# Optimization experiments

Hardware: AMD Instinct MI355X
Metric: run time of the kernel (lower is better)

## Reference

```python
import jax, jax.numpy as jnp
import numpy as np

B, C, P, NP = 16, 768, 2048, 64
FFE = 4


def _ln(x, g, b, eps=1e-5):
    m = jnp.mean(x, axis=-1, keepdims=True)
    v = jnp.mean(jnp.square(x - m), axis=-1, keepdims=True)
    return (x - m) * jax.lax.rsqrt(v + eps) * g + b


def _gelu(x):
    return jax.nn.gelu(x, approximate=False)  # torch nn.GELU default (erf)


def _any_attn(q, k, v, nqg, nqb, nkg, nkb, nvg, nvb, wq, wk, wv, wp, bq, bk, bv, bp):
    # AnyAttention: LN each stream, project, ReLU-gated logits scaled by d^-0.5, softmax, proj
    scale = q.shape[-1] ** -0.5
    qn = _ln(q, nqg, nqb) @ wq + bq
    kn = _ln(k, nkg, nkb) @ wk + bk
    vn = _ln(v, nvg, nvb) @ wv + bv
    attn = jnp.einsum('bqc,bkc->bqk', qn, kn)
    attn = jax.nn.relu(attn) * scale  # returned attn is relu*scale (pre-softmax)
    out = jnp.einsum('bqk,bkc->bqc', jax.nn.softmax(attn, axis=-1), vn)
    return attn, out @ wp + bp


def _forward(x, parts,
             enc_nq_g, enc_nq_b, enc_nk_g, enc_nk_b, enc_nv_g, enc_nv_b,
             enc_wq, enc_wk, enc_wv, enc_wp, enc_bq, enc_bk, enc_bv, enc_bp,
             dec_nq_g, dec_nq_b, dec_nk_g, dec_nk_b, dec_nv_g, dec_nv_b,
             dec_wq, dec_wk, dec_wv, dec_wp, dec_bq, dec_bk, dec_bv, dec_bp,
             ffn_ng, ffn_nb, ffn_w1, ffn_b1, ffn_w2, ffn_b2,
             sr_w1, sr_b1, sr_w2, sr_b2):
    x = jnp.swapaxes(x, 1, 2)  # b c p -> b p c
    # SimpleReasoning: SE-style gate over part tokens (AdaptiveMaxPool1d(1) = max over channel dim)
    g = jnp.max(parts, axis=-1)                                  # [b, np]
    g = _gelu(g @ sr_w1 + sr_b1)
    gate = jax.nn.sigmoid(g @ sr_w2 + sr_b2)[..., None]          # [b, np, 1]
    parts = gate * parts + parts                                 # parts1 + parts (residual)
    # enc_attn: parts attend over image tokens
    attn0, attn_out = _any_attn(parts, x, x,
                                enc_nq_g, enc_nq_b, enc_nk_g, enc_nk_b, enc_nv_g, enc_nv_b,
                                enc_wq, enc_wk, enc_wv, enc_wp, enc_bq, enc_bk, enc_bv, enc_bp)
    attn_0 = jnp.max(attn0, axis=-1)                             # maxpool over k -> [b, np]
    parts_in = parts + attn_out
    # FFN on image tokens with residual
    h = _ln(x, ffn_ng, ffn_nb)
    feats1 = x + (_gelu(h @ ffn_w1 + ffn_b1) @ ffn_w2 + ffn_b2)
    # dec_attn: image tokens attend over part tokens
    _, feats = _any_attn(feats1, parts_in, parts_in,
                         dec_nq_g, dec_nq_b, dec_nk_g, dec_nk_b, dec_nv_g, dec_nv_b,
                         dec_wq, dec_wk, dec_wv, dec_wp, dec_bq, dec_bk, dec_bv, dec_bp)
    feats = x + feats
    return jnp.swapaxes(feats, 1, 2), attn_0                     # [b, c, p], [b, np]


def setup_inputs() -> dict:
    key = jax.random.key(0)
    ki = iter(jax.random.split(key, 48))
    def rn(shape, s=1.0):
        return jax.random.normal(next(ki), shape, jnp.float32) * s
    d = {}
    d['x'] = rn((B, C, P))
    d['parts'] = rn((B, NP, C))
    for pre in ('enc', 'dec'):
        for nm in ('nq', 'nk', 'nv'):
            d[f'{pre}_{nm}_g'] = jnp.ones((C,), jnp.float32)
            d[f'{pre}_{nm}_b'] = jnp.zeros((C,), jnp.float32)
        for nm in ('wq', 'wk', 'wv', 'wp'):
            d[f'{pre}_{nm}'] = rn((C, C), 0.02)
        for nm in ('bq', 'bk', 'bv', 'bp'):
            d[f'{pre}_{nm}'] = jnp.zeros((C,), jnp.float32)
    d['ffn_ng'] = jnp.ones((C,), jnp.float32)
    d['ffn_nb'] = jnp.zeros((C,), jnp.float32)
    d['ffn_w1'] = rn((C, FFE * C), 0.02)
    d['ffn_b1'] = jnp.zeros((FFE * C,), jnp.float32)
    d['ffn_w2'] = rn((FFE * C, C), 0.02)
    d['ffn_b2'] = jnp.zeros((C,), jnp.float32)
    d['sr_w1'] = rn((NP, NP), 0.1)
    d['sr_b1'] = jnp.zeros((NP,), jnp.float32)
    d['sr_w2'] = rn((NP, NP), 0.1)
    d['sr_b2'] = jnp.zeros((NP,), jnp.float32)
    return d


def reference(x, parts,
              enc_nq_g, enc_nq_b, enc_nk_g, enc_nk_b, enc_nv_g, enc_nv_b,
              enc_wq, enc_wk, enc_wv, enc_wp, enc_bq, enc_bk, enc_bv, enc_bp,
              dec_nq_g, dec_nq_b, dec_nk_g, dec_nk_b, dec_nv_g, dec_nv_b,
              dec_wq, dec_wk, dec_wv, dec_wp, dec_bq, dec_bk, dec_bv, dec_bp,
              ffn_ng, ffn_nb, ffn_w1, ffn_b1, ffn_w2, ffn_b2,
              sr_w1, sr_b1, sr_w2, sr_b2):
    return _forward(x, parts,
                    enc_nq_g, enc_nq_b, enc_nk_g, enc_nk_b, enc_nv_g, enc_nv_b,
                    enc_wq, enc_wk, enc_wv, enc_wp, enc_bq, enc_bk, enc_bv, enc_bp,
                    dec_nq_g, dec_nq_b, dec_nk_g, dec_nk_b, dec_nv_g, dec_nv_b,
                    dec_wq, dec_wk, dec_wv, dec_wp, dec_bq, dec_bk, dec_bv, dec_bp,
                    ffn_ng, ffn_nb, ffn_w1, ffn_b1, ffn_w2, ffn_b2,
                    sr_w1, sr_b1, sr_w2, sr_b2)
```

## Files before the change

### kernel.cpp

```cpp
#include <hip/hip_runtime.h>

typedef unsigned short u16;
typedef unsigned int u32;
typedef __bf16 bf16x8 __attribute__((ext_vector_type(8)));
typedef float f32x4 __attribute__((ext_vector_type(4)));
typedef unsigned int u32x4 __attribute__((ext_vector_type(4)));

#define BB 16
#define CC 768
#define PP 2048
#define FF 3072

__device__ __forceinline__ float b2f(u16 u) {
  unsigned int x = ((unsigned int)u) << 16;
  return __builtin_bit_cast(float, x);
}
__device__ __forceinline__ u16 f2b(float f) {
  unsigned int x = __builtin_bit_cast(unsigned int, f);
  x += 0x7fffu + ((x >> 16) & 1u);
  return (u16)(x >> 16);
}
__device__ __forceinline__ float erf_fast(float x) {
  float ax = fabsf(x);
  float t = 1.0f / fmaf(0.3275911f, ax, 1.0f);
  float p = t * fmaf(t, fmaf(t, fmaf(t, fmaf(t, 1.061405429f, -1.453152027f),
                                     1.421413741f), -0.284496736f), 0.254829592f);
  float r = 1.0f - p * __expf(-ax * ax);
  return copysignf(r, x);
}
__device__ __forceinline__ float gelu_f(float x) {
  return 0.5f * x * (1.0f + erf_fast(x * 0.7071067811865475f));
}

typedef __attribute__((address_space(1))) const unsigned int g_u32;
typedef __attribute__((address_space(3))) unsigned int l_u32;
__device__ __forceinline__ void gl_lds16(const u16* g, u16* l) {
  __builtin_amdgcn_global_load_lds((g_u32*)g, (l_u32*)l, 16, 0, 0);
}

struct Wtr10 {
  const float* W[10]; const float* g[10]; u16* O[10];
  int Kd[10]; int Nd[10]; int tr[10]; int cum[11];
};
__global__ void wtr10_k(Wtr10 a) {
  __shared__ float t[64][65];
  int tbid = blockIdx.x;
  int z = 0;
  while (tbid >= a.cum[z + 1]) ++z;
  int r = tbid - a.cum[z];
  const float* W = a.W[z];
  const float* g = a.g[z];
  u16* Wt = a.O[z];
  int K = a.Kd[z], N = a.Nd[z];
  int nbx = N >> 6;
  int n0 = (r % nbx) * 64, k0 = (r / nbx) * 64;
  int tx = threadIdx.x & 63, ty = threadIdx.x >> 6;
  if (!a.tr[z]) {
    for (int i = 0; i < 16; ++i) {
      int k = k0 + ty + i * 4;
      float sc = g ? g[k] : 1.0f;
      Wt[(long)k * N + n0 + tx] = f2b(W[(long)k * N + n0 + tx] * sc);
    }
    return;
  }
  for (int i = 0; i < 16; ++i) {
    int k = k0 + ty + i * 4;
    float sc = g ? g[k] : 1.0f;
    t[ty + i * 4][tx] = W[(long)k * N + n0 + tx] * sc;
  }
  __syncthreads();
  for (int i = 0; i < 16; ++i) {
    int n = n0 + ty + i * 4;
    Wt[(long)n * K + k0 + tx] = f2b(t[tx][ty + i * 4]);
  }
}

struct Bf7 {
  const float* b[7]; const float* nb[7]; const float* W[7]; float* o[7];
  int Kd[7]; int Nd[7];
};
__global__ void bfuse7_k(Bf7 a) {
  __shared__ float red[4][64];
  int tbid = blockIdx.x;
  int z, bx;
  if (tbid < 72) { z = tbid / 12; bx = tbid % 12; }
  else { z = 6; bx = tbid - 72; }
  const float* b = a.b[z];
  const float* nb = a.nb[z];
  const float* W = a.W[z];
  float* outb = a.o[z];
  int K = a.Kd[z], N = a.Nd[z];
  int n = bx * 64 + (threadIdx.x & 63);
  int slice = threadIdx.x >> 6;
  float acc = 0.f;
#pragma unroll 4
  for (int k = slice; k < K; k += 4) acc += nb[k] * W[(long)k * N + n];
  red[slice][threadIdx.x & 63] = acc;
  __syncthreads();
  if (slice == 0)
    outb[n] = b[n] + red[0][threadIdx.x & 63] + red[1][threadIdx.x & 63] +
              red[2][threadIdx.x & 63] + red[3][threadIdx.x & 63];
}

struct Bf2 { const float* b[2]; const float* nb[2]; const float* W[2]; float* o[2]; };
__global__ void bfuse2_k(Bf2 a) {
  __shared__ float red[4][64];
  int z = blockIdx.x / 12, bx = blockIdx.x % 12;
  const float* b = a.b[z];
  const float* nb = a.nb[z];
  const float* W = a.W[z];
  int n = bx * 64 + (threadIdx.x & 63);
  int slice = threadIdx.x >> 6;
  float acc = 0.f;
#pragma unroll 4
  for (int k = slice; k < CC; k += 4) acc += nb[k] * W[(long)k * CC + n];
  red[slice][threadIdx.x & 63] = acc;
  __syncthreads();
  if (slice == 0)
    a.o[z][n] = (b ? b[n] : 0.f) + red[0][threadIdx.x & 63] +
                red[1][threadIdx.x & 63] + red[2][threadIdx.x & 63] +
                red[3][threadIdx.x & 63];
}

struct Dw4 { const u16* A[4]; const float* v[4]; float* o[4]; };
__global__ void dotw4_k(Dw4 a) {
  int z = blockIdx.x / 192;
  int row = (blockIdx.x % 192) * 4 + (threadIdx.x >> 6);
  int lane = threadIdx.x & 63;
  const u16* ip = a.A[z] + (long)row * CC;
  const float* vec = a.v[z];
  float s = 0.f;
  for (int i = 0; i < 12; ++i) s += b2f(ip[lane + i * 64]) * vec[lane + i * 64];
  for (int o = 32; o; o >>= 1) s += __shfl_xor(s, o);
  if (lane == 0) a.o[z][row] = s;
}

__global__ void scal2_k(const float* a0, const float* b0, float* o0,
                        const float* a1, const float* b1, float* o1) {
  int w = threadIdx.x >> 6, lane = threadIdx.x & 63;
  const float* A = w ? a1 : a0;
  const float* Bv = w ? b1 : b0;
  float s = 0.f;
  for (int i = lane; i < CC; i += 64) s += A[i] * Bv[i];
  for (int o = 32; o; o >>= 1) s += __shfl_xor(s, o);
  if (lane == 0) *(w ? o1 : o0) = s;
}

__global__ void dotc_k(const u16* __restrict__ A, const float* __restrict__ vec,
                       const float* __restrict__ cptr, float* __restrict__ outp) {
  int row = blockIdx.x * 4 + (threadIdx.x >> 6);
  int lane = threadIdx.x & 63;
  const u16* ip = A + (long)row * CC;
  float s = 0.f;
  for (int i = 0; i < 12; ++i) s += b2f(ip[lane + i * 64]) * vec[lane + i * 64];
  for (int o = 32; o; o >>= 1) s += __shfl_xor(s, o);
  if (lane == 0) outp[row] = s + cptr[0];
}

__global__ void xprep_k(const float* __restrict__ x, float* __restrict__ mean,
                        float* __restrict__ rstd, u16* __restrict__ xh) {
  __shared__ float t[64][65];
  __shared__ float red[8][64];
  __shared__ float mn_s[64], rs_s[64];
  int p0 = blockIdx.x * 64, b = blockIdx.y;
  int tx = threadIdx.x & 63, ty = threadIdx.x >> 6;
  const float* xb = x + (long)b * CC * PP;
  float s = 0.f, sq = 0.f;
  for (int c = ty; c < CC; c += 4) {
    float f = xb[(long)c * PP + p0 + tx];
    s += f; sq += f * f;
  }
  red[ty][tx] = s;
  red[4 + ty][tx] = sq;
  __syncthreads();
  if (ty == 0) {
    float S = red[0][tx] + red[1][tx] + red[2][tx] + red[3][tx];
    float Q = red[4][tx] + red[5][tx] + red[6][tx] + red[7][tx];
    float m = S * (1.0f / 768.0f);
    float var = Q * (1.0f / 768.0f) - m * m;
    float rs = rsqrtf(var + 1e-5f);
    mn_s[tx] = m; rs_s[tx] = rs;
    int gi = (b << 11) + p0 + tx;
    mean[gi] = m; rstd[gi] = rs;
  }
  __syncthreads();
  u16* ob = xh + (long)b * PP * CC;
  for (int cb = 0; cb < 12; ++cb) {
    int c0 = cb * 64;
    for (int i = 0; i < 16; ++i)
      t[ty + i * 4][tx] = xb[(long)(c0 + ty + i * 4) * PP + p0 + tx];
    __syncthreads();
    for (int i = 0; i < 16; ++i) {
      int pl = ty + i * 4;
      ob[(long)(p0 + pl) * CC + c0 + tx] = f2b((t[tx][pl] - mn_s[pl]) * rs_s[pl]);
    }
    __syncthreads();
  }
}

__global__ void parts_gate_k(const float* __restrict__ parts,
                             const float* __restrict__ w1, const float* __restrict__ b1,
                             const float* __restrict__ w2, const float* __restrict__ b2,
                             float* __restrict__ gate_out) {
  int b = blockIdx.x, t = threadIdx.x;
  __shared__ float g[64], g1[64];
  int r = t >> 2, l4 = t & 3;
  const float* pr = parts + ((long)b * 64 + r) * CC;
  float m = -1e30f;
  for (int c = l4; c < CC; c += 4) m = fmaxf(m, pr[c]);
  m = fmaxf(m, __shfl_xor(m, 1));
  m = fmaxf(m, __shfl_xor(m, 2));
  if (l4 == 0) g[r] = m;
  __syncthreads();
  if (t < 64) {
    float a = b1[t];
    for (int k = 0; k < 64; ++k) a += g[k] * w1[k * 64 + t];
    g1[t] = gelu_f(a);
  }
  __syncthreads();
  if (t < 64) {
    float a = b2[t];
    for (int k = 0; k < 64; ++k) a += g1[k] * w2[k * 64 + t];
    gate_out[b * 64 + t] = 1.0f / (1.0f + expf(-a));
  }
}

__global__ void gate_ln_k(const float* __restrict__ parts, const float* __restrict__ gate,
                          float* __restrict__ parts1, u16* __restrict__ ph) {
  int row = blockIdx.x * 4 + (threadIdx.x >> 6);
  int lane = threadIdx.x & 63;
  float g = 1.0f + gate[row];
  const float* ip = parts + (long)row * CC;
  float* op1 = parts1 + (long)row * CC;
  float v[12];
  float s = 0.f, sq = 0.f;
  for (int i = 0; i < 12; ++i) {
    float f = ip[lane + i * 64] * g;
    v[i] = f; op1[lane + i * 64] = f;
    s += f; sq += f * f;
  }
  for (int o = 32; o; o >>= 1) { s += __shfl_xor(s, o); sq += __shfl_xor(sq, o); }
  float mean = s * (1.0f / 768.0f);
  float var = sq * (1.0f / 768.0f) - mean * mean;
  float rstd = rsqrtf(var + 1e-5f);
  u16* op = ph + (long)row * CC;
  for (int i = 0; i < 12; ++i) op[lane + i * 64] = f2b((v[i] - mean) * rstd);
}

template <typename T>
__global__ void ln_rows_k(const T* __restrict__ in, u16* __restrict__ outp, int rows) {
  int row = blockIdx.x * 4 + (threadIdx.x >> 6);
  if (row >= rows) return;
  int lane = threadIdx.x & 63;
  const T* ip = in + (long)row * CC;
  float v[12];
  float s = 0.f, sq = 0.f;
  for (int i = 0; i < 12; ++i) {
    float f;
    if constexpr (sizeof(T) == 2) f = b2f(((const u16*)ip)[lane + i * 64]);
    else f = ((const float*)ip)[lane + i * 64];
    v[i] = f; s += f; sq += f * f;
  }
  for (int o = 32; o; o >>= 1) { s += __shfl_xor(s, o); sq += __shfl_xor(sq, o); }
  float mean = s * (1.0f / 768.0f);
  float var = sq * (1.0f / 768.0f) - mean * mean;
  float rstd = rsqrtf(var + 1e-5f);
  u16* op = outp + (long)row * CC;
  for (int i = 0; i < 12; ++i) op[lane + i * 64] = f2b((v[i] - mean) * rstd);
}

__global__ void softmax_enc_k(const float* __restrict__ attn, u16* __restrict__ sm,
                              float* __restrict__ attn0) {
  int row = blockIdx.x * 4 + (threadIdx.x >> 6);
  int lane = threadIdx.x & 63;
  const float* ap = attn + (long)row * PP;
  float v[32];
  float m = -1e30f;
  for (int i = 0; i < 32; ++i) { v[i] = ap[lane + i * 64]; m = fmaxf(m, v[i]); }
  for (int o = 32; o; o >>= 1) m = fmaxf(m, __shfl_xor(m, o));
  float s = 0.f;
  for (int i = 0; i < 32; ++i) { float e = expf(v[i] - m); v[i] = e; s += e; }
  for (int o = 32; o; o >>= 1) s += __shfl_xor(s, o);
  float inv = 1.0f / s;
  u16* sp = sm + (long)row * PP;
  for (int i = 0; i < 32; ++i) sp[lane + i * 64] = f2b(v[i] * inv);
  if (lane == 0) attn0[row] = m;
}

__global__ void pvred_k(const float* __restrict__ part, u16* __restrict__ outp) {
  long i = (long)blockIdx.x * 256 + threadIdx.x;
  const f32x4* p = (const f32x4*)part;
  f32x4 a = p[i];
  a += p[i + 196608];
  a += p[i + 2 * 196608];
  a += p[i + 3 * 196608];
  u32 lo = (u32)f2b(a.x) | ((u32)f2b(a.y) << 16);
  u32 hi = (u32)f2b(a.z) | ((u32)f2b(a.w) << 16);
  ((u32*)outp)[i * 2] = lo;
  ((u32*)outp)[i * 2 + 1] = hi;
}

template <int EPI>
__global__ __launch_bounds__(256) void gemmf_k(
    const u16* __restrict__ A, const u16* __restrict__ Bm, void* __restrict__ Cm,
    const float* __restrict__ bias, int M, int N, int K, int lda,
    const float* __restrict__ res32) {
  __shared__ __align__(16) u16 As[128 * 32];
  __shared__ __align__(16) u16 Bs[128 * 32];
  const int nbx = N >> 7;
  const int nwg = gridDim.x;
  int tile = blockIdx.x;
  if ((nwg & 7) == 0) {
    tile = (tile & 7) * (nwg >> 3) + (tile >> 3);
  }
  const int bm0 = (tile / nbx) << 7;
  const int bn0 = (tile % nbx) << 7;
  const int tid = threadIdx.x;
  const int lane = tid & 63;
  const int wave = tid >> 6;
  const int laneq = lane & 15, lanek = lane >> 4;
  const int wm = (wave >> 1) << 6, wn = (wave & 1) << 6;
  const int srow = wave * 32 + (lane >> 2);
  const int scol = (lane & 3) << 3;
  const u16* Ag0 = A + (long)(bm0 + srow) * lda + scol;
  const u16* Ag1 = A + (long)(bm0 + srow + 16) * lda + scol;
  const u16* Bg0 = Bm + (long)(bn0 + srow) * K + scol;
  const u16* Bg1 = Bm + (long)(bn0 + srow + 16) * K + scol;
  u16* lA0 = As + wave * 1024;
  u16* lA1 = As + wave * 1024 + 512;
  u16* lB0 = Bs + wave * 1024;
  u16* lB1 = Bs + wave * 1024 + 512;
  f32x4 acc[4][4] = {};
  for (int k0 = 0; k0 < K; k0 += 32) {
    gl_lds16(Ag0 + k0, lA0);
    gl_lds16(Ag1 + k0, lA1);
    gl_lds16(Bg0 + k0, lB0);
    gl_lds16(Bg1 + k0, lB1);
    __syncthreads();
    bf16x8 af[4], bfr[4];
#pragma unroll
    for (int i = 0; i < 4; ++i)
      af[i] = *(const bf16x8*)(As + (wm + i * 16 + laneq) * 32 + (lanek << 3));
#pragma unroll
    for (int i = 0; i < 4; ++i)
      bfr[i] = *(const bf16x8*)(Bs + (wn + i * 16 + laneq) * 32 + (lanek << 3));
#pragma unroll
    for (int mi = 0; mi < 4; ++mi)
#pragma unroll
      for (int ni = 0; ni < 4; ++ni)
        acc[mi][ni] =
            __builtin_amdgcn_mfma_f32_16x16x32_bf16(af[mi], bfr[ni], acc[mi][ni], 0, 0, 0);
    __syncthreads();
  }
#pragma unroll
  for (int mi = 0; mi < 4; ++mi) {
#pragma unroll
    for (int r = 0; r < 4; ++r) {
      const int row = bm0 + wm + mi * 16 + (lanek << 2) + r;
#pragma unroll
      for (int ni = 0; ni < 4; ++ni) {
        const int col = bn0 + wn + ni * 16 + laneq;
        float v = acc[mi][ni][r] + (bias ? bias[col] : 0.f);
        long off = (long)row * N + col;
        if constexpr (EPI == 0) {
          ((u16*)Cm)[off] = f2b(v);
        } else {
          ((float*)Cm)[off] = v + res32[off];
        }
      }
    }
  }
}

struct G4 { const u16* A[4]; const u16* B[4]; u16* C[4]; };
__global__ __launch_bounds__(256) void gemmf4_k(G4 a) {
  __shared__ __align__(16) u16 As[128 * 32];
  __shared__ __align__(16) u16 Bs[128 * 32];
  const int z = blockIdx.x / 36;
  const int r = blockIdx.x % 36;
  const u16* A = a.A[z];
  const u16* Bm = a.B[z];
  u16* Cm = a.C[z];
  const int bm0 = (r / 6) << 7;
  const int bn0 = (r % 6) << 7;
  const int tid = threadIdx.x;
  const int lane = tid & 63;
  const int wave = tid >> 6;
  const int laneq = lane & 15, lanek = lane >> 4;
  const int wm = (wave >> 1) << 6, wn = (wave & 1) << 6;
  const int srow = wave * 32 + (lane >> 2);
  const int scol = (lane & 3) << 3;
  const u16* Ag0 = A + (long)(bm0 + srow) * CC + scol;
  const u16* Ag1 = A + (long)(bm0 + srow + 16) * CC + scol;
  const u16* Bg0 = Bm + (long)(bn0 + srow) * CC + scol;
  const u16* Bg1 = Bm + (long)(bn0 + srow + 16) * CC + scol;
  u16* lA0 = As + wave * 1024;
  u16* lA1 = As + wave * 1024 + 512;
  u16* lB0 = Bs + wave * 1024;
  u16* lB1 = Bs + wave * 1024 + 512;
  f32x4 acc[4][4] = {};
  for (int k0 = 0; k0 < CC; k0 += 32) {
    gl_lds16(Ag0 + k0, lA0);
    gl_lds16(Ag1 + k0, lA1);
    gl_lds16(Bg0 + k0, lB0);
    gl_lds16(Bg1 + k0, lB1);
    __syncthreads();
    bf16x8 af[4], bfr[4];
#pragma unroll
    for (int i = 0; i < 4; ++i)
      af[i] = *(const bf16x8*)(As + (wm + i * 16 + laneq) * 32 + (lanek << 3));
#pragma unroll
    for (int i = 0; i < 4; ++i)
      bfr[i] = *(const bf16x8*)(Bs + (wn + i * 16 + laneq) * 32 + (lanek << 3));
#pragma unroll
    for (int mi = 0; mi < 4; ++mi)
#pragma unroll
      for (int ni = 0; ni < 4; ++ni)
        acc[mi][ni] =
            __builtin_amdgcn_mfma_f32_16x16x32_bf16(af[mi], bfr[ni], acc[mi][ni], 0, 0, 0);
    __syncthreads();
  }
#pragma unroll
  for (int mi = 0; mi < 4; ++mi)
#pragma unroll
    for (int r2 = 0; r2 < 4; ++r2) {
      const int row = bm0 + wm + mi * 16 + (lanek << 2) + r2;
#pragma unroll
      for (int ni = 0; ni < 4; ++ni) {
        const int col = bn0 + wn + ni * 16 + laneq;
        Cm[(long)row * CC + col] = f2b(acc[mi][ni][r2]);
      }
    }
}

#define G256_BAR() __builtin_amdgcn_s_barrier()
#define G256_WLGKM0()                                    \
  do {                                                   \
    asm volatile("s_waitcnt lgkmcnt(0)" ::: "memory");   \
    __builtin_amdgcn_sched_barrier(0);                   \
  } while (0)
#define G256_RD_A(HALF)                                                        \
  _Pragma("unroll") for (int m2 = 0; m2 < 4; ++m2) {                           \
    af[m2 * 2 + 0] = *(const bf16x8*)(Ab + ar + (HALF)*4096 + m2 * 1024 + g0); \
    af[m2 * 2 + 1] = *(const bf16x8*)(Ab + ar + (HALF)*4096 + m2 * 1024 + g1); \
  }
#define G256_RD_B(HALF, BFR)                                                   \
  _Pragma("unroll") for (int n2 = 0; n2 < 2; ++n2) {                           \
    BFR[n2 * 2 + 0] = *(const bf16x8*)(Bb + br + (HALF)*2048 + n2 * 1024 + g0);\
    BFR[n2 * 2 + 1] = *(const bf16x8*)(Bb + br + (HALF)*2048 + n2 * 1024 + g1);\
  }
#define G256_MFMA_Q(H, NH, BFR)                                                \
  __builtin_amdgcn_s_setprio(1);                                               \
  _Pragma("unroll") for (int m2 = 0; m2 < 4; ++m2)                             \
  _Pragma("unroll") for (int n2 = 0; n2 < 2; ++n2)                             \
  _Pragma("unroll") for (int s = 0; s < 2; ++s)                                \
      acc[(H)*4 + m2][(NH)*2 + n2] = __builtin_amdgcn_mfma_f32_16x16x32_bf16(  \
          af[m2 * 2 + s], BFR[n2 * 2 + s], acc[(H)*4 + m2][(NH)*2 + n2], 0, 0, 0); \
  __builtin_amdgcn_s_setprio(0);

template <int EPI>
__global__ __launch_bounds__(512, 2) void gemm256_k(
    const u16* __restrict__ A, const u16* __restrict__ Bm, void* __restrict__ Cm,
    const float* __restrict__ bias, int M, int N, int K,
    const u16* __restrict__ rxh, const float* __restrict__ rmean,
    const float* __restrict__ rrstd, long rro, int nbm) {
  __shared__ __align__(16) u16 As[2 * 16384];
  __shared__ __align__(16) u16 Bs[2 * 16384];
  const int nbx = N >> 8;
  const int nwg = gridDim.x;
  int tile = blockIdx.x;
  if ((nwg & 7) == 0) {
    tile = (tile & 7) * (nwg >> 3) + (tile >> 3);
  }
  int bm0, bn0;
  if (nbm) {
    bm0 = (tile % nbm) << 8;
    bn0 = (tile / nbm) << 8;
  } else {
    bm0 = (tile / nbx) << 8;
    bn0 = (tile % nbx) << 8;
  }
  const int tid = threadIdx.x;
  const int lane = tid & 63;
  const int wave = tid >> 6;
  const int laneq = lane & 15, lanek = lane >> 4;
  const int wrow = (wave >> 2) << 7;
  const int wcol = (wave & 3) << 6;
  const int srow8 = lane >> 3;
  const int sg = (lane & 7) ^ srow8;
  const u16* gA = A + (long)(bm0 + wave * 8 + srow8) * K + sg * 8;
  const u16* gB = Bm + (long)(bn0 + wave * 8 + srow8) * K + sg * 8;
  const long lineK = (long)64 * K;
  const int ldsLine = wave * 512;
  const int gx = laneq & 7;
  const int g0 = ((lanek) ^ gx) << 3;
  const int g1 = ((lanek + 4) ^ gx) << 3;
  const int ar = (wrow + laneq) * 64;
  const int br = (wcol + laneq) * 64;
  f32x4 acc[8][4] = {};
  bf16x8 af[8], bfr0[4], bfr1[4];
  const int NT = K >> 6;

  {
    u16* dA = (u16*)As;
    u16* dB = (u16*)Bs;
    gl_lds16(gA, dA + ldsLine);
    gl_lds16(gA + lineK, dA + ldsLine + 4096);
    gl_lds16(gA + 2 * lineK, dA + ldsLine + 8192);
    gl_lds16(gA + 3 * lineK, dA + ldsLine + 12288);
    gl_lds16(gB, dB + ldsLine);
    gl_lds16(gB + lineK, dB + ldsLine + 4096);
    gl_lds16(gB + 2 * lineK, dB + ldsLine + 8192);
    gl_lds16(gB + 3 * lineK, dB + ldsLine + 12288);
  }
  for (int T = 0; T < NT; ++T) {
    const u16* Ab = As + (T & 1) * 16384;
    const u16* Bb = Bs + (T & 1) * 16384;
    u16* An = (u16*)As + ((T & 1) ^ 1) * 16384;
    u16* Bn = (u16*)Bs + ((T & 1) ^ 1) * 16384;
    const long ko = (long)(T + 1) * 64;
    const bool more = (T + 1 < NT);
    if (more) {
      gl_lds16(gA + ko, An + ldsLine);
      gl_lds16(gA + ko + lineK, An + ldsLine + 4096);
      gl_lds16(gB + ko, Bn + ldsLine);
      gl_lds16(gB + ko + lineK, Bn + ldsLine + 4096);
      asm volatile("s_waitcnt vmcnt(4)" ::: "memory");
    } else {
      asm volatile("s_waitcnt vmcnt(0)" ::: "memory");
    }
    G256_BAR();
    G256_RD_A(0);
    G256_RD_B(0, bfr0);
    G256_WLGKM0();
    G256_MFMA_Q(0, 0, bfr0);
    G256_BAR();
    if (more) {
      gl_lds16(gA + ko + 2 * lineK, An + ldsLine + 8192);
      gl_lds16(gA + ko + 3 * lineK, An + ldsLine + 12288);
      gl_lds16(gB + ko + 2 * lineK, Bn + ldsLine + 8192);
      gl_lds16(gB + ko + 3 * lineK, Bn + ldsLine + 12288);
    }
    G256_RD_B(1, bfr1);
    G256_BAR();
    G256_WLGKM0();
    G256_MFMA_Q(0, 1, bfr1);
    G256_BAR();
    G256_RD_A(1);
    G256_BAR();
    G256_WLGKM0();
    G256_MFMA_Q(1, 1, bfr1);
    G256_BAR();
    G256_MFMA_Q(1, 0, bfr0);
  }

#pragma unroll
  for (int mi = 0; mi < 8; ++mi) {
#pragma unroll
    for (int r = 0; r < 4; ++r) {
      const int row = bm0 + wrow + mi * 16 + (lanek << 2) + r;
      float mn = 0.f, istd = 0.f;
      if constexpr (EPI == 3) {
        long gr = rro + row;
        mn = rmean[gr];
        istd = 1.0f / rrstd[gr];
      }
#pragma unroll
      for (int ni = 0; ni < 4; ++ni) {
        const int col = bn0 + wcol + ni * 16 + laneq;
        float v = acc[mi][ni][r] + bias[col];
        long off = (long)row * N + col;
        if constexpr (EPI == 0) {
          ((u16*)Cm)[off] = f2b(v);
        } else if constexpr (EPI == 1) {
          ((u16*)Cm)[off] = f2b(gelu_f(v));
        } else {
          v += b2f(rxh[(rro + row) * 768 + col]) * istd + mn;
          ((u16*)Cm)[off] = f2b(v);
        }
      }
    }
  }
}

template <int EPI, bool BNT, int TM, int TN>
__global__ __launch_bounds__(256) void gemm_k(
    const u16* __restrict__ A, const u16* __restrict__ Bm, void* __restrict__ Cm,
    const float* __restrict__ bias, int M, int N, int kLen, int lda, int ldB,
    long sA, long sB, long sC, float scale, const float* __restrict__ res32,
    const float* __restrict__ radd) {
  __shared__ __align__(16) u16 As[TM][40];
  __shared__ __align__(16) u16 Bs[TN][40];
  const int bn0 = blockIdx.x * TN;
  const int bm0 = (EPI == 4) ? 0 : blockIdx.y * TM;
  const int kOff = (EPI == 4) ? blockIdx.y * kLen : 0;
  const int bz = blockIdx.z;
  const u16* Ab = A + (long)bz * sA;
  const u16* Bb = Bm + (long)bz * sB;
  const long coff = (EPI == 4) ? ((long)blockIdx.y * gridDim.z + bz) * sC
                               : (long)bz * sC;
  const int tid = threadIdx.x;
  const int lane = tid & 63;
  const int wave = tid >> 6;
  const int wm = (TM == 64) ? 0 : ((TN == 64) ? wave * 32 : ((wave >> 1) << 6));
  const int wn = (TN == 64) ? 0 : ((TM == 64) ? wave * 32 : ((wave & 1) << 6));
  constexpr int MI = (TN == 64) ? 2 : 4;
  constexpr int NI = (TM == 64) ? 2 : 4;
  const int laneq = lane & 15, lanek = lane >> 4;
  f32x4 acc[MI][NI] = {};
  for (int k0 = 0; k0 < kLen; k0 += 32) {
    __syncthreads();
#pragma unroll
    for (int j = 0; j < TM / 64; ++j) {
      int v = tid + j * 256;
      int m = v >> 2, kcl = (v & 3) << 3;
      u32x4 val = {0, 0, 0, 0};
      if (bm0 + m < M)
        val = *(const u32x4*)(Ab + (long)(bm0 + m) * lda + kOff + k0 + kcl);
      *(u32x4*)(&As[m][kcl]) = val;
    }
    if constexpr (BNT) {
#pragma unroll
      for (int j = 0; j < TN / 64; ++j) {
        int v = tid + j * 256;
        int n = v >> 2, kcl = (v & 3) << 3;
        u32x4 val = {0, 0, 0, 0};
        if (bn0 + n < N)
          val = *(const u32x4*)(Bb + (long)(bn0 + n) * ldB + kOff + k0 + kcl);
        *(u32x4*)(&Bs[n][kcl]) = val;
      }
    } else {
      constexpr int CCH = TN / 8;
#pragma unroll
      for (int j = 0; j < TN / 64; ++j) {
        int v = tid + j * 256;
        int kk = v / CCH, nc = (v % CCH) << 3;
        u32x4 val = {0, 0, 0, 0};
        if (bn0 + nc < N)
          val = *(const u32x4*)(Bb + (long)(kOff + k0 + kk) * ldB + bn0 + nc);
        union { u32x4 v4; u16 u[8]; } uu;
        uu.v4 = val;
#pragma unroll
        for (int e = 0; e < 8; ++e) Bs[nc + e][kk] = uu.u[e];
      }
    }
    __syncthreads();
    bf16x8 af[MI], bfr[NI];
#pragma unroll
    for (int i = 0; i < MI; ++i)
      af[i] = *(const bf16x8*)(&As[wm + i * 16 + laneq][lanek << 3]);
#pragma unroll
    for (int i = 0; i < NI; ++i)
      bfr[i] = *(const bf16x8*)(&Bs[wn + i * 16 + laneq][lanek << 3]);
#pragma unroll
    for (int mi = 0; mi < MI; ++mi)
#pragma unroll
      for (int ni = 0; ni < NI; ++ni)
        acc[mi][ni] =
            __builtin_amdgcn_mfma_f32_16x16x32_bf16(af[mi], bfr[ni], acc[mi][ni], 0, 0, 0);
  }
  if constexpr (EPI == 5) {
    __syncthreads();
    float* smem = (float*)(wave < 2 ? (void*)As : (void*)Bs) + (wave & 1) * 1024;
    const int pbase = bm0 + wm + (lane & 3) * 16;
    const long obase = (long)bz * CC * PP;
#pragma unroll
    for (int ni = 0; ni < 4; ++ni) {
#pragma unroll
      for (int mi = 0; mi < 4; ++mi)
#pragma unroll
        for (int r = 0; r < 4; ++r) {
          const int col = bn0 + wn + ni * 16 + laneq;
          smem[(mi * 16 + (lanek << 2) + r) * 16 + laneq] = acc[mi][ni][r] + bias[col];
        }
      const int c = bn0 + wn + ni * 16 + (lane >> 2);
      const float* xs = res32 + obase + (long)c * PP + pbase;
      float* os = (float*)Cm + obase + (long)c * PP + pbase;
      const float* sr = smem + (lane & 3) * 256 + (lane >> 2);
#pragma unroll
      for (int q4 = 0; q4 < 4; ++q4) {
        f32x4 xv = *(const f32x4*)(xs + q4 * 4);
        f32x4 ov;
        ov.x = sr[(q4 * 4 + 0) * 16] + xv.x;
        ov.y = sr[(q4 * 4 + 1) * 16] + xv.y;
        ov.z = sr[(q4 * 4 + 2) * 16] + xv.z;
        ov.w = sr[(q4 * 4 + 3) * 16] + xv.w;
        *(f32x4*)(os + q4 * 4) = ov;
      }
    }
  } else if constexpr (EPI == 6) {
#pragma unroll
    for (int mi = 0; mi < MI; ++mi) {
#pragma unroll
      for (int r = 0; r < 4; ++r) {
        float e[NI];
        float mx = -1e30f;
#pragma unroll
        for (int ni = 0; ni < NI; ++ni) {
          const int col = bn0 + wn + ni * 16 + laneq;
          float v = acc[mi][ni][r] + (radd ? radd[(long)bz * N + col] : 0.f);
          v = fmaxf(v, 0.0f) * scale;
          e[ni] = v;
          mx = fmaxf(mx, v);
        }
        mx = fmaxf(mx, __shfl_xor(mx, 1));
        mx = fmaxf(mx, __shfl_xor(mx, 2));
        mx = fmaxf(mx, __shfl_xor(mx, 4));
        mx = fmaxf(mx, __shfl_xor(mx, 8));
        float s = 0.f;
#pragma unroll
        for (int ni = 0; ni < NI; ++ni) { e[ni] = __expf(e[ni] - mx); s += e[ni]; }
        s += __shfl_xor(s, 1);
        s += __shfl_xor(s, 2);
        s += __shfl_xor(s, 4);
        s += __shfl_xor(s, 8);
        float inv = 1.0f / s;
        const int row = bm0 + wm + mi * 16 + (lanek << 2) + r;
#pragma unroll
        for (int ni = 0; ni < NI; ++ni) {
          const int col = bn0 + wn + ni * 16 + laneq;
          ((u16*)Cm)[coff + (long)row * N + col] = f2b(e[ni] * inv);
        }
      }
    }
  } else {
#pragma unroll
    for (int mi = 0; mi < MI; ++mi) {
#pragma unroll
      for (int ni = 0; ni < NI; ++ni) {
        int col = bn0 + wn + ni * 16 + laneq;
        if (col >= N) continue;
#pragma unroll
        for (int r = 0; r < 4; ++r) {
          int row = bm0 + wm + mi * 16 + (lanek << 2) + r;
          if (row >= M) continue;
          float v = acc[mi][ni][r];
          long off = coff + (long)row * N + col;
          if constexpr (EPI == 2) {
            v += radd ? radd[(long)bz * M + row] : 0.f;
            ((float*)Cm)[off] = fmaxf(v, 0.0f) * scale;
          } else {
            ((float*)Cm)[off] = v;
          }
        }
      }
    }
  }
}

extern "C" void kernel_launch(void* const* d_in, const int* in_sizes, int n_in,
                              void* d_out, int out_size, void* d_ws, size_t ws_size,
                              hipStream_t stream) {
  (void)in_sizes; (void)n_in; (void)out_size;
  const float* x        = (const float*)d_in[0];
  const float* parts    = (const float*)d_in[1];
  const float* enc_nq_g = (const float*)d_in[2];
  const float* enc_nq_b = (const float*)d_in[3];
  const float* enc_nk_g = (const float*)d_in[4];
  const float* enc_nk_b = (const float*)d_in[5];
  const float* enc_nv_g = (const float*)d_in[6];
  const float* enc_nv_b = (const float*)d_in[7];
  const float* enc_wq   = (const float*)d_in[8];
  const float* enc_wk   = (const float*)d_in[9];
  const float* enc_wv   = (const float*)d_in[10];
  const float* enc_wp   = (const float*)d_in[11];
  const float* enc_bq   = (const float*)d_in[12];
  const float* enc_bk   = (const float*)d_in[13];
  const float* enc_bv   = (const float*)d_in[14];
  const float* enc_bp   = (const float*)d_in[15];
  const float* dec_nq_g = (const float*)d_in[16];
  const float* dec_nq_b = (const float*)d_in[17];
  const float* dec_nk_g = (const float*)d_in[18];
  const float* dec_nk_b = (const float*)d_in[19];
  const float* dec_nv_g = (const float*)d_in[20];
  const float* dec_nv_b = (const float*)d_in[21];
  const float* dec_wq   = (const float*)d_in[22];
  const float* dec_wk   = (const float*)d_in[23];
  const float* dec_wv   = (const float*)d_in[24];
  const float* dec_wp   = (const float*)d_in[25];
  const float* dec_bq   = (const float*)d_in[26];
  const float* dec_bk   = (const float*)d_in[27];
  const float* dec_bv   = (const float*)d_in[28];
  const float* dec_bp   = (const float*)d_in[29];
  const float* ffn_ng   = (const float*)d_in[30];
  const float* ffn_nb   = (const float*)d_in[31];
  const float* ffn_w1   = (const float*)d_in[32];
  const float* ffn_b1   = (const float*)d_in[33];
  const float* ffn_w2   = (const float*)d_in[34];
  const float* ffn_b2   = (const float*)d_in[35];
  const float* sr_w1    = (const float*)d_in[36];
  const float* sr_b1    = (const float*)d_in[37];
  const float* sr_w2    = (const float*)d_in[38];
  const float* sr_b2    = (const float*)d_in[39];
  float* outp = (float*)d_out;

  char* base = (char*)d_ws;
  size_t used = 0;
  auto alloc = [&](size_t bytes) -> void* {
    void* p = base + used;
    used += (bytes + 255) & ~(size_t)255;
    return p;
  };
  const long MC = (long)CC * CC;
  u16* WpeT = (u16*)alloc(MC * 2);
  u16* WpdT = (u16*)alloc(MC * 2);
  u16* W1T  = (u16*)alloc((long)CC * FF * 2);
  u16* W2T  = (u16*)alloc((long)CC * FF * 2);
  u16* WkR  = (u16*)alloc(MC * 2);
  u16* WqR  = (u16*)alloc(MC * 2);
  u16* WvS  = (u16*)alloc(MC * 2);
  u16* WqdR = (u16*)alloc(MC * 2);
  u16* WkdR = (u16*)alloc(MC * 2);
  u16* WvdR = (u16*)alloc(MC * 2);
  u16* m2w  = (u16*)alloc(MC * 2);
  u16* Bqk  = (u16*)alloc(MC * 2);
  u16* Bg   = (u16*)alloc(MC * 2);
  u16* Bv   = (u16*)alloc(MC * 2);
  float* bqe  = (float*)alloc(CC * 4);
  float* bke  = (float*)alloc(CC * 4);
  float* bve  = (float*)alloc(CC * 4);
  float* bqd  = (float*)alloc(CC * 4);
  float* bkd  = (float*)alloc(CC * 4);
  float* bvd  = (float*)alloc(CC * 4);
  float* b1f  = (float*)alloc(FF * 4);
  float* bias2   = (float*)alloc(CC * 4);
  float* bias_vw = (float*)alloc(CC * 4);
  float* bq2     = (float*)alloc(CC * 4);
  float* wqb     = (float*)alloc(CC * 4);
  float* bias_g  = (float*)alloc(CC * 4);
  float* wkb     = (float*)alloc(CC * 4);
  float* cq      = (float*)alloc(256);
  float* ck      = (float*)alloc(256);
  float* meanx = (float*)alloc((long)BB * PP * 4);
  float* rstdx = (float*)alloc((long)BB * PP * 4);
  const long BPC = (long)BB * PP * CC;
  u16* bufA = (u16*)alloc(BPC * 2);
  u16* bufB = (u16*)alloc(BPC * 2);
  const long PC = (long)BB * 64 * CC;
  float* parts1   = (float*)alloc(PC * 4);
  float* gateb    = (float*)alloc((long)BB * 64 * 4);
  u16*   p1hat    = (u16*)alloc(PC * 2);
  u16*   qtil     = (u16*)alloc(PC * 2);
  float* qdotv    = (float*)alloc((long)BB * 64 * 4);
  float* attn_e   = (float*)alloc((long)BB * 64 * PP * 4);
  u16*   sm_e     = (u16*)alloc((long)BB * 64 * PP * 2);
  u16*   pv_e     = (u16*)alloc(PC * 2);
  float* pvpart   = (float*)alloc((long)4 * PC * 4);
  float* parts_in = (float*)alloc(PC * 4);
  u16*   pin_hat  = (u16*)alloc(PC * 2);
  u16*   Gm       = (u16*)alloc(PC * 2);
  u16*   VW       = (u16*)alloc(PC * 2);
  float* kdotv    = (float*)alloc((long)BB * 64 * 4);
  u16*   sm_d     = (u16*)alloc((long)BB * PP * 64 * 2);
  int chunk_rows = 16384;
  while (chunk_rows > 4096 &&
         used + (size_t)chunk_rows * FF * 2 > ws_size)
    chunk_rows >>= 1;
  u16* ff1 = (u16*)alloc((long)chunk_rows * FF * 2);
  if (used > ws_size) return;

  const float scale = 0.03608439182435161f;
  dim3 blk(256);
  dim3 blk2(512);

  {
    Wtr10 wa;
    const float* Ws[10] = {enc_wp, dec_wp, ffn_w1, ffn_w2, enc_wk,
                           enc_wq, enc_wv, dec_wq, dec_wk, dec_wv};
    const float* gs[10] = {nullptr, nullptr, ffn_ng, nullptr, enc_nk_g,
                           enc_nq_g, enc_nv_g, dec_nq_g, dec_nk_g, dec_nv_g};
    u16* Os[10] = {WpeT, WpdT, W1T, W2T, WkR, WqR, WvS, WqdR, WkdR, WvdR};
    int Ks[10] = {CC, CC, CC, FF, CC, CC, CC, CC, CC, CC};
    int Ns[10] = {CC, CC, FF, CC, CC, CC, CC, CC, CC, CC};
    int tr[10] = {1, 1, 1, 1, 0, 0, 0, 0, 0, 0};
    int cum = 0;
    for (int i = 0; i < 10; ++i) {
      wa.W[i] = Ws[i]; wa.g[i] = gs[i]; wa.O[i] = Os[i];
      wa.Kd[i] = Ks[i]; wa.Nd[i] = Ns[i]; wa.tr[i] = tr[i];
      wa.cum[i] = cum;
      cum += (Ns[i] / 64) * (Ks[i] / 64);
    }
    wa.cum[10] = cum;
    wtr10_k<<<cum, blk, 0, stream>>>(wa);
    Bf7 ba;
    const float* bs[7] = {enc_bq, enc_bk, enc_bv, dec_bq, dec_bk, dec_bv, ffn_b1};
    const float* nbs[7] = {enc_nq_b, enc_nk_b, enc_nv_b, dec_nq_b, dec_nk_b,
                           dec_nv_b, ffn_nb};
    const float* ws[7] = {enc_wq, enc_wk, enc_wv, dec_wq, dec_wk, dec_wv, ffn_w1};
    float* os[7] = {bqe, bke, bve, bqd, bkd, bvd, b1f};
    for (int i = 0; i < 7; ++i) {
      ba.b[i] = bs[i]; ba.nb[i] = nbs[i]; ba.W[i] = ws[i]; ba.o[i] = os[i];
      ba.Kd[i] = CC; ba.Nd[i] = (i == 6) ? FF : CC;
    }
    bfuse7_k<<<120, blk, 0, stream>>>(ba);
    Bf2 b2a;
    b2a.b[0] = enc_bp;  b2a.nb[0] = bve; b2a.W[0] = enc_wp; b2a.o[0] = bias2;
    b2a.b[1] = nullptr; b2a.nb[1] = bvd; b2a.W[1] = dec_wp; b2a.o[1] = bias_vw;
    bfuse2_k<<<24, blk, 0, stream>>>(b2a);
    Dw4 da;
    da.A[0] = WkR;  da.v[0] = bqe; da.o[0] = bq2;
    da.A[1] = WqR;  da.v[1] = bke; da.o[1] = wqb;
    da.A[2] = WqdR; da.v[2] = bkd; da.o[2] = bias_g;
    da.A[3] = WkdR; da.v[3] = bqd; da.o[3] = wkb;
    dotw4_k<<<768, blk, 0, stream>>>(da);
    scal2_k<<<1, 128, 0, stream>>>(bqe, bke, cq, bkd, bqd, ck);
    G4 ga;
    ga.A[0] = WpeT; ga.B[0] = WvS;  ga.C[0] = m2w;
    ga.A[1] = WkR;  ga.B[1] = WqR;  ga.C[1] = Bqk;
    ga.A[2] = WqdR; ga.B[2] = WkdR; ga.C[2] = Bg;
    ga.A[3] = WpdT; ga.B[3] = WvdR; ga.C[3] = Bv;
    gemmf4_k<<<144, blk, 0, stream>>>(ga);
  }

  xprep_k<<<dim3(32, 16), blk, 0, stream>>>(x, meanx, rstdx, bufA);

  parts_gate_k<<<16, blk, 0, stream>>>(parts, sr_w1, sr_b1, sr_w2, sr_b2, gateb);
  gate_ln_k<<<256, blk, 0, stream>>>(parts, gateb, parts1, p1hat);

  gemmf_k<0><<<48, blk, 0, stream>>>(p1hat, Bqk, qtil, bq2, 1024, CC, CC, CC,
      nullptr);
  dotc_k<<<256, blk, 0, stream>>>(p1hat, wqb, cq, qdotv);

  gemm_k<2, true, 64, 128><<<dim3(16, 1, 16), blk, 0, stream>>>(
      qtil, bufA, attn_e, nullptr, 64, PP, CC, CC, CC,
      (long)64 * CC, (long)PP * CC, (long)64 * PP, scale, nullptr, qdotv);
  softmax_enc_k<<<256, blk, 0, stream>>>(attn_e, sm_e, outp + (long)BB * CC * PP);
  gemm_k<4, false, 64, 128><<<dim3(6, 4, 16), blk, 0, stream>>>(
      sm_e, bufA, pvpart, nullptr, 64, CC, PP / 4, PP, CC,
      (long)64 * PP, (long)PP * CC, (long)64 * CC, 0.f, nullptr, nullptr);
  pvred_k<<<768, blk, 0, stream>>>(pvpart, pv_e);
  gemmf_k<4><<<48, blk, 0, stream>>>(pv_e, m2w, parts_in, bias2, 1024, CC, CC, CC,
      parts1);

  ln_rows_k<float><<<256, blk, 0, stream>>>(parts_in, pin_hat, 1024);
  gemmf_k<0><<<48, blk, 0, stream>>>(pin_hat, Bg, Gm, bias_g, 1024, CC, CC, CC,
      nullptr);
  gemmf_k<0><<<48, blk, 0, stream>>>(pin_hat, Bv, VW, bias_vw, 1024, CC, CC, CC,
      nullptr);
  dotc_k<<<256, blk, 0, stream>>>(pin_hat, wkb, ck, kdotv);

  for (long r0 = 0; r0 < 32768; r0 += chunk_rows) {
    gemm256_k<1><<<(chunk_rows / 256) * 12, blk2, 0, stream>>>(
        bufA + r0 * CC, W1T, ff1, b1f, chunk_rows, FF, CC,
        nullptr, nullptr, nullptr, 0, chunk_rows / 256);
    gemm256_k<3><<<(chunk_rows / 256) * 3, blk2, 0, stream>>>(
        ff1, W2T, bufB + r0 * CC, ffn_b2, chunk_rows, CC, FF,
        bufA, meanx, rstdx, r0, 0);
  }
  ln_rows_k<u16><<<8192, blk, 0, stream>>>(bufB, bufB, 32768);

  gemm_k<6, true, 128, 64><<<dim3(1, 16, 16), blk, 0, stream>>>(
      bufB, Gm, sm_d, nullptr, PP, 64, CC, CC, CC,
      (long)PP * CC, (long)64 * CC, (long)PP * 64, scale, nullptr, kdotv);

  gemm_k<5, false, 128, 128><<<dim3(6, 16, 16), blk, 0, stream>>>(
      sm_d, VW, outp, dec_bp, PP, CC, 64, 64, CC,
      (long)PP * 64, (long)64 * CC, 0, 0.f, x, nullptr);
}
```

Measured before the change: 1.070 ms.

## Merge decoder G/V projections into one GEMM and use gemmf for FFN1

Concatenates the Bg and Bv weight matrices and their biases so the two decoder projections of pin_hat run as one 1024x1536 GEMM launch. Downstream kernels read the interleaved GVW buffer through a doubled leading dimension. Separately, the FFN first GEMM moves from the 256-tile gemm256_k kernel to the 128-tile gemmf_k, which gains a new GELU epilogue. This trades tile size for more blocks on the largest GEMM, which may lower per-block data reuse.

```diff
diff --git a/kernel.cpp b/kernel.cpp
--- a/kernel.cpp
+++ b/kernel.cpp
@@ -364,6 +364,8 @@
         long off = (long)row * N + col;
         if constexpr (EPI == 0) {
           ((u16*)Cm)[off] = f2b(v);
+        } else if constexpr (EPI == 1) {
+          ((u16*)Cm)[off] = f2b(gelu_f(v));
         } else {
           ((float*)Cm)[off] = v + res32[off];
         }
@@ -814,8 +816,7 @@
   u16* WvdR = (u16*)alloc(MC * 2);
   u16* m2w  = (u16*)alloc(MC * 2);
   u16* Bqk  = (u16*)alloc(MC * 2);
-  u16* Bg   = (u16*)alloc(MC * 2);
-  u16* Bv   = (u16*)alloc(MC * 2);
+  u16* Bgv  = (u16*)alloc(MC * 2 * 2);
   float* bqe  = (float*)alloc(CC * 4);
   float* bke  = (float*)alloc(CC * 4);
   float* bve  = (float*)alloc(CC * 4);
@@ -824,10 +825,9 @@
   float* bvd  = (float*)alloc(CC * 4);
   float* b1f  = (float*)alloc(FF * 4);
   float* bias2   = (float*)alloc(CC * 4);
-  float* bias_vw = (float*)alloc(CC * 4);
+  float* bias_gv = (float*)alloc(2 * CC * 4);
   float* bq2     = (float*)alloc(CC * 4);
   float* wqb     = (float*)alloc(CC * 4);
-  float* bias_g  = (float*)alloc(CC * 4);
   float* wkb     = (float*)alloc(CC * 4);
   float* cq      = (float*)alloc(256);
   float* ck      = (float*)alloc(256);
@@ -848,8 +848,7 @@
   float* pvpart   = (float*)alloc((long)4 * PC * 4);
   float* parts_in = (float*)alloc(PC * 4);
   u16*   pin_hat  = (u16*)alloc(PC * 2);
-  u16*   Gm       = (u16*)alloc(PC * 2);
-  u16*   VW       = (u16*)alloc(PC * 2);
+  u16*   GVW      = (u16*)alloc(PC * 2 * 2);
   float* kdotv    = (float*)alloc((long)BB * 64 * 4);
   u16*   sm_d     = (u16*)alloc((long)BB * PP * 64 * 2);
   int chunk_rows = 16384;
@@ -895,20 +894,20 @@
     bfuse7_k<<<120, blk, 0, stream>>>(ba);
     Bf2 b2a;
     b2a.b[0] = enc_bp;  b2a.nb[0] = bve; b2a.W[0] = enc_wp; b2a.o[0] = bias2;
-    b2a.b[1] = nullptr; b2a.nb[1] = bvd; b2a.W[1] = dec_wp; b2a.o[1] = bias_vw;
+    b2a.b[1] = nullptr; b2a.nb[1] = bvd; b2a.W[1] = dec_wp; b2a.o[1] = bias_gv + CC;
     bfuse2_k<<<24, blk, 0, stream>>>(b2a);
     Dw4 da;
     da.A[0] = WkR;  da.v[0] = bqe; da.o[0] = bq2;
     da.A[1] = WqR;  da.v[1] = bke; da.o[1] = wqb;
-    da.A[2] = WqdR; da.v[2] = bkd; da.o[2] = bias_g;
+    da.A[2] = WqdR; da.v[2] = bkd; da.o[2] = bias_gv;
     da.A[3] = WkdR; da.v[3] = bqd; da.o[3] = wkb;
     dotw4_k<<<768, blk, 0, stream>>>(da);
     scal2_k<<<1, 128, 0, stream>>>(bqe, bke, cq, bkd, bqd, ck);
     G4 ga;
     ga.A[0] = WpeT; ga.B[0] = WvS;  ga.C[0] = m2w;
     ga.A[1] = WkR;  ga.B[1] = WqR;  ga.C[1] = Bqk;
-    ga.A[2] = WqdR; ga.B[2] = WkdR; ga.C[2] = Bg;
-    ga.A[3] = WpdT; ga.B[3] = WvdR; ga.C[3] = Bv;
+    ga.A[2] = WqdR; ga.B[2] = WkdR; ga.C[2] = Bgv;
+    ga.A[3] = WpdT; ga.B[3] = WvdR; ga.C[3] = Bgv + MC;
     gemmf4_k<<<144, blk, 0, stream>>>(ga);
   }
 
@@ -933,16 +932,13 @@
       parts1);
 
   ln_rows_k<float><<<256, blk, 0, stream>>>(parts_in, pin_hat, 1024);
-  gemmf_k<0><<<48, blk, 0, stream>>>(pin_hat, Bg, Gm, bias_g, 1024, CC, CC, CC,
-      nullptr);
-  gemmf_k<0><<<48, blk, 0, stream>>>(pin_hat, Bv, VW, bias_vw, 1024, CC, CC, CC,
-      nullptr);
+  gemmf_k<0><<<96, blk, 0, stream>>>(pin_hat, Bgv, GVW, bias_gv, 1024, 2 * CC, CC,
+      CC, nullptr);
   dotc_k<<<256, blk, 0, stream>>>(pin_hat, wkb, ck, kdotv);
 
   for (long r0 = 0; r0 < 32768; r0 += chunk_rows) {
-    gemm256_k<1><<<(chunk_rows / 256) * 12, blk2, 0, stream>>>(
-        bufA + r0 * CC, W1T, ff1, b1f, chunk_rows, FF, CC,
-        nullptr, nullptr, nullptr, 0, chunk_rows / 256);
+    gemmf_k<1><<<(chunk_rows / 128) * 24, blk, 0, stream>>>(
+        bufA + r0 * CC, W1T, ff1, b1f, chunk_rows, FF, CC, CC, nullptr);
     gemm256_k<3><<<(chunk_rows / 256) * 3, blk2, 0, stream>>>(
         ff1, W2T, bufB + r0 * CC, ffn_b2, chunk_rows, CC, FF,
         bufA, meanx, rstdx, r0, 0);
@@ -950,10 +946,10 @@
   ln_rows_k<u16><<<8192, blk, 0, stream>>>(bufB, bufB, 32768);
 
   gemm_k<6, true, 128, 64><<<dim3(1, 16, 16), blk, 0, stream>>>(
-      bufB, Gm, sm_d, nullptr, PP, 64, CC, CC, CC,
-      (long)PP * CC, (long)64 * CC, (long)PP * 64, scale, nullptr, kdotv);
+      bufB, GVW, sm_d, nullptr, PP, 64, CC, CC, 2 * CC,
+      (long)PP * CC, (long)64 * 2 * CC, (long)PP * 64, scale, nullptr, kdotv);
 
   gemm_k<5, false, 128, 128><<<dim3(6, 16, 16), blk, 0, stream>>>(
-      sm_d, VW, outp, dec_bp, PP, CC, 64, 64, CC,
-      (long)PP * 64, (long)64 * CC, 0, 0.f, x, nullptr);
-}
+      sm_d, GVW + CC, outp, dec_bp, PP, CC, 64, 64, 2 * CC,
+      (long)PP * 64, (long)64 * 2 * CC, 0, 0.f, x, nullptr);
+}
```

After: 1.077 ms. No clear change (+0.7%).
